# Kernel optimization log

Hardware: AMD Instinct MI355X
Metric: run time of the kernel (lower is better)

Reference implementation:

```python
import jax, jax.numpy as jnp
import numpy as np

SCALES = (0, 1, 2, 3)
SIGMA_NSQ = 2.0
SIGMA_MAX_INV = 4.0 / (255.0 * 255.0)
GAIN_LIMIT = 100.0  # NEG=False
EPS = 1e-10


def gaussian_kernel_2d(N):
    sigma = N / 5.0
    x = jnp.arange(N, dtype=jnp.float32) - (N - 1) / 2.0
    g = jnp.exp(-(x * x) / (2.0 * sigma * sigma))
    k = jnp.outer(g, g)
    return (k / jnp.sum(k))[None, None]  # [1,1,N,N]


def reflect_pad(x, p):
    return jnp.pad(x, ((0, 0), (0, 0), (p, p), (p, p)), mode='reflect')


def conv2d(x, w, stride=1, groups=1):
    return jax.lax.conv_general_dilated(
        x, w, (stride, stride), 'VALID',
        dimension_numbers=('NCHW', 'OIHW', 'NCHW'),
        feature_group_count=groups)


def vif_num_den(ref, dist):
    ref = ref - 128.0
    dist = dist - 128.0
    h, w = ref.shape[-2], ref.shape[-1]
    nums, dens = [], []
    for scale in SCALES:
        N = 2 ** (4 - scale) + 1
        win = gaussian_kernel_2d(N)
        p = (N - 1) // 2
        if scale > 0:
            h, w = h // 2, w // 2
            ref = conv2d(reflect_pad(ref, p), win, stride=2)[:, :, :h, :w]
            dist = conv2d(reflect_pad(dist, p), win, stride=2)[:, :, :h, :w]
        win5 = jnp.tile(win, (5, 1, 1, 1))  # grouped conv, 5 channels
        inp = jnp.concatenate([ref, dist, ref * ref, dist * dist, ref * dist], axis=1)
        out = conv2d(reflect_pad(inp, p), win5, groups=5)  # [b,5,h,w]
        mu1, mu2, s1, s2, s12 = [out[:, i:i + 1] for i in range(5)]
        s1 = jax.nn.relu(s1 - mu1 * mu1)
        s2 = jax.nn.relu(s2 - mu2 * mu2)
        s12 = s12 - mu1 * mu2
        g = s12 / (s1 + EPS)
        sv = s2 - g * s12
        m1 = s1 < EPS
        g = jnp.where(m1, 0.0, g)
        sv = jnp.where(m1, s2, sv)
        s1 = jnp.where(m1, 0.0, s1)
        m2 = s2 < EPS
        g = jnp.where(m2, 0.0, g)
        sv = jnp.where(m2, 0.0, sv)
        sv = jnp.where(g < 0.0, s2, sv)
        g = jax.nn.relu(g)
        sv = jnp.where(sv <= EPS, EPS, sv)
        g = jnp.minimum(g, GAIN_LIMIT)
        num_ar = jnp.log2(1.0 + g * g * s1 / (sv + SIGMA_NSQ))
        den_ar = jnp.log2(1.0 + s1 / SIGMA_NSQ)
        num_ar = jnp.where(s12 < 0.0, 0.0, num_ar)
        m3 = s1 < SIGMA_NSQ
        num_ar = jnp.where(m3, 1.0 - s2 * SIGMA_MAX_INV, num_ar)
        den_ar = jnp.where(m3, 1.0, den_ar)
        nums.append(jnp.sum(num_ar, axis=(-1, -2, -3)))
        dens.append(jnp.sum(den_ar, axis=(-1, -2, -3)))
    return jnp.stack(nums, axis=-1), jnp.stack(dens, axis=-1)


def setup_inputs() -> dict:
    key = jax.random.key(0)
    k1, k2 = jax.random.split(key)
    shape = (4, 1, 1080, 1920)
    ref = jax.random.uniform(k1, shape, dtype=jnp.float32) * 255.0
    dist = jax.random.uniform(k2, shape, dtype=jnp.float32) * 255.0
    return {"ref": ref, "dist": dist}


def reference(ref, dist):
    num, den = vif_num_den(ref, dist)
    return num / den  # VIF features per scale, shape [b, 4]
```

## Files before the change

kernel.cpp:

```cpp
#include <hip/hip_runtime.h>
#include <math.h>

#define VIF_EPS       1e-10f
#define SIGMA_NSQ     2.0f
#define SIGMA_MAX_INV (4.0f / (255.0f * 255.0f))
#define GAIN_LIMIT    100.0f

typedef float v2f __attribute__((ext_vector_type(2)));
typedef float v4f __attribute__((ext_vector_type(4)));

static __device__ __forceinline__ v2f splat2(float s) {
    v2f v; v.x = s; v.y = s; return v;
}

__device__ __forceinline__ int reflect_idx(int i, int n) {
    i = (i < 0) ? -i : i;
    i = (i >= n) ? (2 * n - 2 - i) : i;
    return i;
}

template <int N>
__device__ __forceinline__ void compute_weights(float* wts) {
    if (threadIdx.x == 0) {
        const float sigma = (float)N / 5.0f;
        const float denom = 2.0f * sigma * sigma;
        float s = 0.0f;
        for (int i = 0; i < N; ++i) {
            float x = (float)i - (float)(N - 1) * 0.5f;
            float g = expf(-(x * x) / denom);
            wts[i] = g;
            s += g;
        }
        for (int i = 0; i < N; ++i) wts[i] = wts[i] / s;
    }
}

constexpr int tile_w(int N) { return (128 - (N - 1)) & ~3; }

template <int N>
struct alignas(16) StatsSmem {
    v2f   a[8][132];
    v2f   bq[8][132];
    float c[8][132];
    float wts[N];
    float rsum[8];
};
template <int N>
struct alignas(16) DownSmem {
    v2f vb[8][252];
    float wts[N];
};

template <int N>
__device__ __forceinline__ void stats_body(
    StatsSmem<N>& sm, const float* __restrict__ refp, const float* __restrict__ distp,
    int h, int w, float shift, double2* __restrict__ partial,
    int sy, int sx, int bx, int b) {
    constexpr int P   = (N - 1) / 2;
    constexpr int VC  = 128;
    constexpr int TW  = tile_w(N);
    constexpr int TH  = 8;
    constexpr int Q   = 4;
    constexpr int LR  = Q + 2 * P;
    constexpr int XG  = TW / 4;

    const int tid = threadIdx.x;
    const int ytile = bx % sy;
    const int xtile = bx / sy;
    const int x0 = xtile * TW;
    const int y0 = ytile * TH;

    compute_weights<N>(sm.wts);
    __syncthreads();

    float wr[N];
#pragma unroll
    for (int j = 0; j < N; ++j) wr[j] = sm.wts[j];

    {
        const int cc = tid & (VC - 1);
        const int g  = tid >> 7;
        const int gx = reflect_idx(x0 + cc - P, w);
        const float* rb = refp  + (size_t)b * h * w + gx;
        const float* db = distp + (size_t)b * h * w + gx;

        v2f accA[Q], accB[Q];
        float accC[Q];
#pragma unroll
        for (int q = 0; q < Q; ++q) {
            accA[q] = splat2(0.f);
            accB[q] = splat2(0.f);
            accC[q] = 0.f;
        }

        auto acc_push = [&](int i, float r, float d) {
            v2f rd; rd.x = r; rd.y = d;
            v2f sq = rd * rd;
            float x = r * d;
#pragma unroll
            for (int q = 0; q < Q; ++q) {
                const int j = i - q;
                if (j >= 0 && j < N) {
                    const float wj = wr[j];
                    accA[q] += splat2(wj) * rd;
                    accB[q] += splat2(wj) * sq;
                    accC[q] += wj * x;
                }
            }
        };

        const int rowlo = y0 + g * Q - P;
        if (rowlo >= 0 && rowlo + LR <= h) {
            const float* pr = rb + (size_t)rowlo * w;
            const float* pd = db + (size_t)rowlo * w;
#pragma unroll
            for (int i = 0; i < LR; ++i) {
                float r = pr[0] - shift;
                float d = pd[0] - shift;
                pr += w; pd += w;
                acc_push(i, r, d);
            }
        } else {
#pragma unroll
            for (int i = 0; i < LR; ++i) {
                int gy = reflect_idx(rowlo + i, h);
                float r = rb[(size_t)gy * w] - shift;
                float d = db[(size_t)gy * w] - shift;
                acc_push(i, r, d);
            }
        }
#pragma unroll
        for (int q = 0; q < Q; ++q) {
            sm.a[g * Q + q][cc]  = accA[q];
            sm.bq[g * Q + q][cc] = accB[q];
            sm.c[g * Q + q][cc]  = accC[q];
        }
    }
    __syncthreads();

    float num_v = 0.f, den_v = 0.f;
    {
        const int xg  = tid & 31;
        const int row = tid >> 5;
        if (xg < XG) {
            constexpr int WC  = N + 3;
            constexpr int F4C = (WC + 3) / 4;

            v2f muA[4], muB[4];
            float muC[4];
#pragma unroll
            for (int q = 0; q < 4; ++q) {
                muA[q] = splat2(0.f);
                muB[q] = splat2(0.f);
                muC[q] = 0.f;
            }

            const v4f* A4 = (const v4f*)&sm.a[row][xg * 4];
            const v4f* B4 = (const v4f*)&sm.bq[row][xg * 4];
#pragma unroll
            for (int f = 0; f < WC / 2; ++f) {
                v4f ta = A4[f];
                v4f tb = B4[f];
#pragma unroll
                for (int hlf = 0; hlf < 2; ++hlf) {
                    const int k = 2 * f + hlf;
                    v2f pa = hlf ? __builtin_shufflevector(ta, ta, 2, 3)
                                 : __builtin_shufflevector(ta, ta, 0, 1);
                    v2f pb = hlf ? __builtin_shufflevector(tb, tb, 2, 3)
                                 : __builtin_shufflevector(tb, tb, 0, 1);
#pragma unroll
                    for (int q = 0; q < 4; ++q) {
                        const int j = k - q;
                        if (j >= 0 && j < N) {
                            const float wj = wr[j];
                            muA[q] += splat2(wj) * pa;
                            muB[q] += splat2(wj) * pb;
                        }
                    }
                }
            }
            {
                const v4f* C4 = (const v4f*)&sm.c[row][xg * 4];
#pragma unroll
                for (int f = 0; f < F4C; ++f) {
                    v4f t = C4[f];
#pragma unroll
                    for (int e = 0; e < 4; ++e) {
                        const int k = 4 * f + e;
                        const float x = (e == 0) ? t.x : (e == 1) ? t.y
                                      : (e == 2) ? t.z : t.w;
#pragma unroll
                        for (int q = 0; q < 4; ++q) {
                            const int j = k - q;
                            if (j >= 0 && j < N) muC[q] += wr[j] * x;
                        }
                    }
                }
            }

            const int gy = y0 + row;
#pragma unroll
            for (int q = 0; q < 4; ++q) {
                int gx = x0 + xg * 4 + q;
                if (gx < w && gy < h) {
                    float mu1 = muA[q].x, mu2 = muA[q].y;
                    float s1  = fmaxf(0.f, muB[q].x - mu1 * mu1);
                    float s2  = fmaxf(0.f, muB[q].y - mu2 * mu2);
                    float s12 = muC[q] - mu1 * mu2;

                    float g  = s12 / (s1 + VIF_EPS);
                    float sv = s2 - g * s12;
                    if (s1 < VIF_EPS) { g = 0.f; sv = s2; s1 = 0.f; }
                    if (s2 < VIF_EPS) { g = 0.f; sv = 0.f; }
                    if (g  < 0.f)     { sv = s2; g = 0.f; }
                    if (sv <= VIF_EPS) sv = VIF_EPS;
                    g = fminf(g, GAIN_LIMIT);

                    float num_ar = __log2f(1.f + g * g * s1 / (sv + SIGMA_NSQ));
                    float den_ar = __log2f(1.f + s1 / SIGMA_NSQ);
                    if (s12 < 0.f) num_ar = 0.f;
                    if (s1 < SIGMA_NSQ) { num_ar = 1.f - s2 * SIGMA_MAX_INV; den_ar = 1.f; }
                    num_v += num_ar;
                    den_v += den_ar;
                }
            }
        }
    }

#pragma unroll
    for (int off = 32; off > 0; off >>= 1) {
        num_v += __shfl_down(num_v, off);
        den_v += __shfl_down(den_v, off);
    }
    const int wid = tid >> 6, lane = tid & 63;
    if (lane == 0) { sm.rsum[wid] = num_v; sm.rsum[4 + wid] = den_v; }
    __syncthreads();
    if (tid == 0) {
        float ns = sm.rsum[0] + sm.rsum[1] + sm.rsum[2] + sm.rsum[3];
        float ds = sm.rsum[4] + sm.rsum[5] + sm.rsum[6] + sm.rsum[7];
        partial[(size_t)b * (sy * sx) + bx] = make_double2((double)ns, (double)ds);
    }
}

template <int N>
__device__ __forceinline__ void down_body(
    DownSmem<N>& sm, const float* __restrict__ rin, const float* __restrict__ din,
    float* __restrict__ rout, float* __restrict__ dout,
    int h, int w, int h2, int w2, float shift, int dgx, int bx, int b) {
    constexpr int P   = (N - 1) / 2;
    constexpr int TOW = 120, TOH = 8;
    constexpr int IC  = 2 * (TOW - 1) + N;
    constexpr int NR  = 2 * (TOH - 1) + N;
    constexpr int XG4 = TOW / 4;
    constexpr int WL  = N + 6;

    compute_weights<N>(sm.wts);
    __syncthreads();

    float wr[N];
#pragma unroll
    for (int j = 0; j < N; ++j) wr[j] = sm.wts[j];

    const int tid = threadIdx.x;
    const int xt  = bx % dgx;
    const int yt  = bx / dgx;
    const int x0  = xt * TOW;
    const int y0  = yt * TOH;

    if (tid < IC) {
        const int gx = reflect_idx(2 * x0 - P + tid, w);
        const int rowlo = 2 * y0 - P;
        const float* rb = rin + (size_t)b * h * w + gx;
        const float* db = din + (size_t)b * h * w + gx;

        v2f acc[TOH];
#pragma unroll
        for (int t = 0; t < TOH; ++t) acc[t] = splat2(0.f);

        const bool interior = (rowlo >= 0) && (rowlo + NR <= h);
        if (interior) {
            const float* pr = rb + (size_t)rowlo * w;
            const float* pd = db + (size_t)rowlo * w;
#pragma unroll
            for (int i = 0; i < NR; ++i) {
                v2f x; x.x = pr[0] - shift; x.y = pd[0] - shift;
                pr += w; pd += w;
#pragma unroll
                for (int t = 0; t < TOH; ++t) {
                    const int j = i - 2 * t;
                    if (j >= 0 && j < N) acc[t] += splat2(wr[j]) * x;
                }
            }
        } else {
#pragma unroll
            for (int i = 0; i < NR; ++i) {
                const int gy = reflect_idx(rowlo + i, h);
                v2f x; x.x = rb[(size_t)gy * w] - shift; x.y = db[(size_t)gy * w] - shift;
#pragma unroll
                for (int t = 0; t < TOH; ++t) {
                    const int j = i - 2 * t;
                    if (j >= 0 && j < N) acc[t] += splat2(wr[j]) * x;
                }
            }
        }
#pragma unroll
        for (int t = 0; t < TOH; ++t) sm.vb[t][tid] = acc[t];
    }
    __syncthreads();

    if (tid < TOH * XG4) {
        const int row = tid / XG4;
        const int xg  = tid - row * XG4;

        v2f o[4];
#pragma unroll
        for (int q = 0; q < 4; ++q) o[q] = splat2(0.f);

        const v4f* s4 = (const v4f*)&sm.vb[row][8 * xg];
#pragma unroll
        for (int f = 0; f < (WL + 1) / 2; ++f) {
            v4f t = s4[f];
#pragma unroll
            for (int hlf = 0; hlf < 2; ++hlf) {
                const int k = 2 * f + hlf;
                v2f p = hlf ? __builtin_shufflevector(t, t, 2, 3)
                            : __builtin_shufflevector(t, t, 0, 1);
#pragma unroll
                for (int q = 0; q < 4; ++q) {
                    const int j = k - 2 * q;
                    if (j >= 0 && j < N) o[q] += splat2(wr[j]) * p;
                }
            }
        }
        const int gy = y0 + row;
        if (gy < h2) {
            float* rp = rout + (size_t)b * h2 * w2 + (size_t)gy * w2 + x0 + 4 * xg;
            float* dp = dout + (size_t)b * h2 * w2 + (size_t)gy * w2 + x0 + 4 * xg;
            *(float4*)rp = make_float4(o[0].x, o[1].x, o[2].x, o[3].x);
            *(float4*)dp = make_float4(o[0].y, o[1].y, o[2].y, o[3].y);
        }
    }
}

template <int NS, int ND>
__global__ __launch_bounds__(256) void fused_kernel(
    const float* __restrict__ sref, const float* __restrict__ sdist,
    int sh, int sw, float sshift, double2* __restrict__ partial, int sy, int sx,
    float* __restrict__ drout, float* __restrict__ ddout,
    int dh2, int dw2, int dgx, int nStats) {
    __shared__ union {
        StatsSmem<NS> s;
        DownSmem<ND>  d;
    } u;
    const int bx = blockIdx.x;
    const int b  = blockIdx.z;
    if (bx < nStats)
        stats_body<NS>(u.s, sref, sdist, sh, sw, sshift, partial, sy, sx, bx, b);
    else
        down_body<ND>(u.d, sref, sdist, drout, ddout, sh, sw, dh2, dw2, sshift, dgx,
                      bx - nStats, b);
}

template <int N>
__global__ __launch_bounds__(256) void stats_only_kernel(
    const float* __restrict__ refp, const float* __restrict__ distp,
    int h, int w, float shift, double2* __restrict__ partial, int sy, int sx) {
    __shared__ StatsSmem<N> sm;
    stats_body<N>(sm, refp, distp, h, w, shift, partial, sy, sx, blockIdx.x, blockIdx.z);
}

__global__ __launch_bounds__(256) void reduce_kernel(
    const double2* __restrict__ part, float* __restrict__ out,
    int4 bases, int4 counts) {
    __shared__ double sn[4], sd[4];
    const int s = blockIdx.x & 3;
    const int b = blockIdx.x >> 2;
    const int base = (&bases.x)[s];
    const int cnt  = (&counts.x)[s];
    const double2* p = part + base + (size_t)b * cnt;

    double ns = 0.0, ds = 0.0;
    for (int i = threadIdx.x; i < cnt; i += 256) {
        double2 v = p[i];
        ns += v.x;
        ds += v.y;
    }
#pragma unroll
    for (int off = 32; off > 0; off >>= 1) {
        ns += __shfl_down(ns, off);
        ds += __shfl_down(ds, off);
    }
    const int wid = threadIdx.x >> 6, lane = threadIdx.x & 63;
    if (lane == 0) { sn[wid] = ns; sd[wid] = ds; }
    __syncthreads();
    if (threadIdx.x == 0) {
        double Nv = sn[0] + sn[1] + sn[2] + sn[3];
        double Dv = sd[0] + sd[1] + sd[2] + sd[3];
        out[b * 4 + s] = (float)(Nv / Dv);
    }
}

extern "C" void kernel_launch(void* const* d_in, const int* in_sizes, int n_in,
                              void* d_out, int out_size, void* d_ws, size_t ws_size,
                              hipStream_t stream) {
    const float* ref  = (const float*)d_in[0];
    const float* dist = (const float*)d_in[1];
    float* out = (float*)d_out;

    const int B = 4;
    const int H0 = 1080, W0 = 1920;
    const int H1 = 540,  W1 = 960;
    const int H2 = 270,  W2 = 480;
    const int H3 = 135,  W3 = 240;

    char*  ws  = (char*)d_ws;
    size_t off = 0;
    auto alloc = [&](size_t bytes) -> void* {
        void* p = ws + off;
        off += (bytes + 255) & ~(size_t)255;
        return p;
    };
    float* ref1  = (float*)alloc((size_t)B * H1 * W1 * 4);
    float* dist1 = (float*)alloc((size_t)B * H1 * W1 * 4);
    float* ref2  = (float*)alloc((size_t)B * H2 * W2 * 4);
    float* dist2 = (float*)alloc((size_t)B * H2 * W2 * 4);
    float* ref3  = (float*)alloc((size_t)B * H3 * W3 * 4);
    float* dist3 = (float*)alloc((size_t)B * H3 * W3 * 4);

    const int sx0 = (W0 + tile_w(17) - 1) / tile_w(17), sy0 = (H0 + 7) / 8;
    const int sx1 = (W1 + tile_w(9)  - 1) / tile_w(9),  sy1 = (H1 + 7) / 8;
    const int sx2 = (W2 + tile_w(5)  - 1) / tile_w(5),  sy2 = (H2 + 7) / 8;
    const int sx3 = (W3 + tile_w(3)  - 1) / tile_w(3),  sy3 = (H3 + 7) / 8;
    const int n0 = sx0 * sy0, n1 = sx1 * sy1, n2 = sx2 * sy2, n3 = sx3 * sy3;

    const int dgx1 = W1 / 120, nD1 = dgx1 * ((H1 + 7) / 8);
    const int dgx2 = W2 / 120, nD2 = dgx2 * ((H2 + 7) / 8);
    const int dgx3 = W3 / 120, nD3 = dgx3 * ((H3 + 7) / 8);

    double2* part = (double2*)alloc((size_t)B * (n0 + n1 + n2 + n3) * sizeof(double2));
    double2* p0 = part;
    double2* p1 = p0 + (size_t)B * n0;
    double2* p2 = p1 + (size_t)B * n1;
    double2* p3 = p2 + (size_t)B * n2;

    dim3 blk(256);

    fused_kernel<17, 9><<<dim3(n0 + nD1, 1, B), blk, 0, stream>>>(
        ref, dist, H0, W0, 128.0f, p0, sy0, sx0,
        ref1, dist1, H1, W1, dgx1, n0);

    fused_kernel<9, 5><<<dim3(n1 + nD2, 1, B), blk, 0, stream>>>(
        ref1, dist1, H1, W1, 0.0f, p1, sy1, sx1,
        ref2, dist2, H2, W2, dgx2, n1);

    fused_kernel<5, 3><<<dim3(n2 + nD3, 1, B), blk, 0, stream>>>(
        ref2, dist2, H2, W2, 0.0f, p2, sy2, sx2,
        ref3, dist3, H3, W3, dgx3, n2);

    stats_only_kernel<3><<<dim3(n3, 1, B), blk, 0, stream>>>(
        ref3, dist3, H3, W3, 0.0f, p3, sy3, sx3);

    reduce_kernel<<<16, 256, 0, stream>>>(
        part, out,
        make_int4(0, B * n0, B * (n0 + n1), B * (n0 + n1 + n2)),
        make_int4(n0, n1, n2, n3));
}
```

Measured before the change: 193.3 us.

## Widen stats tile to 256 columns with one thread per column over all rows

The stats kernel's tile grows from 128 to 256 columns. Each of the 256 threads now runs the vertical pass for one column across all 8 output rows, where before two row-groups of 4 each re-read their own halo rows. This cuts redundant global halo loads per tile, both vertically and horizontally, at the cost of more accumulator registers and larger shared memory. The horizontal pass loops over tasks when they exceed 256, and global addressing switches to 32-bit byte offsets from a base pointer in both kernels so the loads can use cheaper offset arithmetic.

Result: faster. 188.2 us (-2.6%).

```diff
diff --git a/kernel.cpp b/kernel.cpp
--- a/kernel.cpp
+++ b/kernel.cpp
@@ -35,13 +35,13 @@
     }
 }
 
-constexpr int tile_w(int N) { return (128 - (N - 1)) & ~3; }
+constexpr int tile_w(int N) { return (256 - (N - 1)) & ~3; }
 
 template <int N>
 struct alignas(16) StatsSmem {
-    v2f   a[8][132];
-    v2f   bq[8][132];
-    float c[8][132];
+    v2f   a[8][258];
+    v2f   bq[8][258];
+    float c[8][260];
     float wts[N];
     float rsum[8];
 };
@@ -57,12 +57,12 @@
     int h, int w, float shift, double2* __restrict__ partial,
     int sy, int sx, int bx, int b) {
     constexpr int P   = (N - 1) / 2;
-    constexpr int VC  = 128;
     constexpr int TW  = tile_w(N);
     constexpr int TH  = 8;
-    constexpr int Q   = 4;
-    constexpr int LR  = Q + 2 * P;
-    constexpr int XG  = TW / 4;
+    constexpr int LR  = TH + 2 * P;
+    constexpr int XG4 = TW / 4;
+    constexpr int NT  = TH * XG4;
+    constexpr int REPS = (NT + 255) / 256;
 
     const int tid = threadIdx.x;
     const int ytile = bx % sy;
@@ -78,19 +78,18 @@
     for (int j = 0; j < N; ++j) wr[j] = sm.wts[j];
 
     {
-        const int cc = tid & (VC - 1);
-        const int g  = tid >> 7;
+        const int cc = tid;
         const int gx = reflect_idx(x0 + cc - P, w);
-        const float* rb = refp  + (size_t)b * h * w + gx;
-        const float* db = distp + (size_t)b * h * w + gx;
-
-        v2f accA[Q], accB[Q];
-        float accC[Q];
-#pragma unroll
-        for (int q = 0; q < Q; ++q) {
-            accA[q] = splat2(0.f);
-            accB[q] = splat2(0.f);
-            accC[q] = 0.f;
+        const float* rbase = refp  + (size_t)b * h * w;
+        const float* dbase = distp + (size_t)b * h * w;
+
+        v2f accA[TH], accB[TH];
+        float accC[TH];
+#pragma unroll
+        for (int t = 0; t < TH; ++t) {
+            accA[t] = splat2(0.f);
+            accB[t] = splat2(0.f);
+            accC[t] = 0.f;
         }
 
         auto acc_push = [&](int i, float r, float d) {
@@ -98,130 +97,135 @@
             v2f sq = rd * rd;
             float x = r * d;
 #pragma unroll
-            for (int q = 0; q < Q; ++q) {
-                const int j = i - q;
+            for (int t = 0; t < TH; ++t) {
+                const int j = i - t;
                 if (j >= 0 && j < N) {
                     const float wj = wr[j];
-                    accA[q] += splat2(wj) * rd;
-                    accB[q] += splat2(wj) * sq;
-                    accC[q] += wj * x;
+                    accA[t] += splat2(wj) * rd;
+                    accB[t] += splat2(wj) * sq;
+                    accC[t] += wj * x;
                 }
             }
         };
 
-        const int rowlo = y0 + g * Q - P;
+        const int rowlo = y0 - P;
         if (rowlo >= 0 && rowlo + LR <= h) {
-            const float* pr = rb + (size_t)rowlo * w;
-            const float* pd = db + (size_t)rowlo * w;
+            unsigned voff = (unsigned)(rowlo * w + gx) * 4u;
+            const unsigned vstep = (unsigned)w * 4u;
 #pragma unroll
             for (int i = 0; i < LR; ++i) {
-                float r = pr[0] - shift;
-                float d = pd[0] - shift;
-                pr += w; pd += w;
+                float r = *(const float*)((const char*)rbase + voff) - shift;
+                float d = *(const float*)((const char*)dbase + voff) - shift;
+                voff += vstep;
                 acc_push(i, r, d);
             }
         } else {
 #pragma unroll
             for (int i = 0; i < LR; ++i) {
-                int gy = reflect_idx(rowlo + i, h);
-                float r = rb[(size_t)gy * w] - shift;
-                float d = db[(size_t)gy * w] - shift;
+                const int gy = reflect_idx(rowlo + i, h);
+                const size_t o = (size_t)gy * w + gx;
+                float r = rbase[o] - shift;
+                float d = dbase[o] - shift;
                 acc_push(i, r, d);
             }
         }
 #pragma unroll
-        for (int q = 0; q < Q; ++q) {
-            sm.a[g * Q + q][cc]  = accA[q];
-            sm.bq[g * Q + q][cc] = accB[q];
-            sm.c[g * Q + q][cc]  = accC[q];
+        for (int t = 0; t < TH; ++t) {
+            sm.a[t][cc]  = accA[t];
+            sm.bq[t][cc] = accB[t];
+            sm.c[t][cc]  = accC[t];
         }
     }
     __syncthreads();
 
     float num_v = 0.f, den_v = 0.f;
     {
-        const int xg  = tid & 31;
-        const int row = tid >> 5;
-        if (xg < XG) {
-            constexpr int WC  = N + 3;
-            constexpr int F4C = (WC + 3) / 4;
-
-            v2f muA[4], muB[4];
-            float muC[4];
-#pragma unroll
-            for (int q = 0; q < 4; ++q) {
-                muA[q] = splat2(0.f);
-                muB[q] = splat2(0.f);
-                muC[q] = 0.f;
-            }
-
-            const v4f* A4 = (const v4f*)&sm.a[row][xg * 4];
-            const v4f* B4 = (const v4f*)&sm.bq[row][xg * 4];
-#pragma unroll
-            for (int f = 0; f < WC / 2; ++f) {
-                v4f ta = A4[f];
-                v4f tb = B4[f];
-#pragma unroll
-                for (int hlf = 0; hlf < 2; ++hlf) {
-                    const int k = 2 * f + hlf;
-                    v2f pa = hlf ? __builtin_shufflevector(ta, ta, 2, 3)
-                                 : __builtin_shufflevector(ta, ta, 0, 1);
-                    v2f pb = hlf ? __builtin_shufflevector(tb, tb, 2, 3)
-                                 : __builtin_shufflevector(tb, tb, 0, 1);
-#pragma unroll
-                    for (int q = 0; q < 4; ++q) {
-                        const int j = k - q;
-                        if (j >= 0 && j < N) {
-                            const float wj = wr[j];
-                            muA[q] += splat2(wj) * pa;
-                            muB[q] += splat2(wj) * pb;
+        constexpr int WC  = N + 3;
+        constexpr int F4C = (WC + 3) / 4;
+#pragma unroll
+        for (int rep = 0; rep < REPS; ++rep) {
+            const int task = tid + 256 * rep;
+            if (task < NT) {
+                const int row = task / XG4;
+                const int xg  = task - row * XG4;
+
+                v2f muA[4], muB[4];
+                float muC[4];
+#pragma unroll
+                for (int q = 0; q < 4; ++q) {
+                    muA[q] = splat2(0.f);
+                    muB[q] = splat2(0.f);
+                    muC[q] = 0.f;
+                }
+
+                const v4f* A4 = (const v4f*)&sm.a[row][xg * 4];
+                const v4f* B4 = (const v4f*)&sm.bq[row][xg * 4];
+#pragma unroll
+                for (int f = 0; f < WC / 2; ++f) {
+                    v4f ta = A4[f];
+                    v4f tb = B4[f];
+#pragma unroll
+                    for (int hlf = 0; hlf < 2; ++hlf) {
+                        const int k = 2 * f + hlf;
+                        v2f pa = hlf ? __builtin_shufflevector(ta, ta, 2, 3)
+                                     : __builtin_shufflevector(ta, ta, 0, 1);
+                        v2f pb = hlf ? __builtin_shufflevector(tb, tb, 2, 3)
+                                     : __builtin_shufflevector(tb, tb, 0, 1);
+#pragma unroll
+                        for (int q = 0; q < 4; ++q) {
+                            const int j = k - q;
+                            if (j >= 0 && j < N) {
+                                const float wj = wr[j];
+                                muA[q] += splat2(wj) * pa;
+                                muB[q] += splat2(wj) * pb;
+                            }
                         }
                     }
                 }
-            }
-            {
-                const v4f* C4 = (const v4f*)&sm.c[row][xg * 4];
-#pragma unroll
-                for (int f = 0; f < F4C; ++f) {
-                    v4f t = C4[f];
-#pragma unroll
-                    for (int e = 0; e < 4; ++e) {
-                        const int k = 4 * f + e;
-                        const float x = (e == 0) ? t.x : (e == 1) ? t.y
-                                      : (e == 2) ? t.z : t.w;
-#pragma unroll
-                        for (int q = 0; q < 4; ++q) {
-                            const int j = k - q;
-                            if (j >= 0 && j < N) muC[q] += wr[j] * x;
+                {
+                    const v4f* C4 = (const v4f*)&sm.c[row][xg * 4];
+#pragma unroll
+                    for (int f = 0; f < F4C; ++f) {
+                        v4f t = C4[f];
+#pragma unroll
+                        for (int e = 0; e < 4; ++e) {
+                            const int k = 4 * f + e;
+                            const float x = (e == 0) ? t.x : (e == 1) ? t.y
+                                          : (e == 2) ? t.z : t.w;
+#pragma unroll
+                            for (int q = 0; q < 4; ++q) {
+                                const int j = k - q;
+                                if (j >= 0 && j < N) muC[q] += wr[j] * x;
+                            }
                         }
                     }
                 }
-            }
-
-            const int gy = y0 + row;
-#pragma unroll
-            for (int q = 0; q < 4; ++q) {
-                int gx = x0 + xg * 4 + q;
-                if (gx < w && gy < h) {
-                    float mu1 = muA[q].x, mu2 = muA[q].y;
-                    float s1  = fmaxf(0.f, muB[q].x - mu1 * mu1);
-                    float s2  = fmaxf(0.f, muB[q].y - mu2 * mu2);
-                    float s12 = muC[q] - mu1 * mu2;
-
-                    float g  = s12 / (s1 + VIF_EPS);
-                    float sv = s2 - g * s12;
-                    if (s1 < VIF_EPS) { g = 0.f; sv = s2; s1 = 0.f; }
-                    if (s2 < VIF_EPS) { g = 0.f; sv = 0.f; }
-                    if (g  < 0.f)     { sv = s2; g = 0.f; }
-                    if (sv <= VIF_EPS) sv = VIF_EPS;
-                    g = fminf(g, GAIN_LIMIT);
-
-                    float num_ar = __log2f(1.f + g * g * s1 / (sv + SIGMA_NSQ));
-                    float den_ar = __log2f(1.f + s1 / SIGMA_NSQ);
-                    if (s12 < 0.f) num_ar = 0.f;
-                    if (s1 < SIGMA_NSQ) { num_ar = 1.f - s2 * SIGMA_MAX_INV; den_ar = 1.f; }
-                    num_v += num_ar;
-                    den_v += den_ar;
+
+                const int gy = y0 + row;
+#pragma unroll
+                for (int q = 0; q < 4; ++q) {
+                    int gx = x0 + xg * 4 + q;
+                    if (gx < w && gy < h) {
+                        float mu1 = muA[q].x, mu2 = muA[q].y;
+                        float s1  = fmaxf(0.f, muB[q].x - mu1 * mu1);
+                        float s2  = fmaxf(0.f, muB[q].y - mu2 * mu2);
+                        float s12 = muC[q] - mu1 * mu2;
+
+                        float g  = s12 / (s1 + VIF_EPS);
+                        float sv = s2 - g * s12;
+                        if (s1 < VIF_EPS) { g = 0.f; sv = s2; s1 = 0.f; }
+                        if (s2 < VIF_EPS) { g = 0.f; sv = 0.f; }
+                        if (g  < 0.f)     { sv = s2; g = 0.f; }
+                        if (sv <= VIF_EPS) sv = VIF_EPS;
+                        g = fminf(g, GAIN_LIMIT);
+
+                        float num_ar = __log2f(1.f + g * g * s1 / (sv + SIGMA_NSQ));
+                        float den_ar = __log2f(1.f + s1 / SIGMA_NSQ);
+                        if (s12 < 0.f) num_ar = 0.f;
+                        if (s1 < SIGMA_NSQ) { num_ar = 1.f - s2 * SIGMA_MAX_INV; den_ar = 1.f; }
+                        num_v += num_ar;
+                        den_v += den_ar;
+                    }
                 }
             }
         }
@@ -270,8 +274,8 @@
     if (tid < IC) {
         const int gx = reflect_idx(2 * x0 - P + tid, w);
         const int rowlo = 2 * y0 - P;
-        const float* rb = rin + (size_t)b * h * w + gx;
-        const float* db = din + (size_t)b * h * w + gx;
+        const float* rbase = rin + (size_t)b * h * w;
+        const float* dbase = din + (size_t)b * h * w;
 
         v2f acc[TOH];
 #pragma unroll
@@ -279,12 +283,14 @@
 
         const bool interior = (rowlo >= 0) && (rowlo + NR <= h);
         if (interior) {
-            const float* pr = rb + (size_t)rowlo * w;
-            const float* pd = db + (size_t)rowlo * w;
+            unsigned voff = (unsigned)(rowlo * w + gx) * 4u;
+            const unsigned vstep = (unsigned)w * 4u;
 #pragma unroll
             for (int i = 0; i < NR; ++i) {
-                v2f x; x.x = pr[0] - shift; x.y = pd[0] - shift;
-                pr += w; pd += w;
+                v2f x;
+                x.x = *(const float*)((const char*)rbase + voff) - shift;
+                x.y = *(const float*)((const char*)dbase + voff) - shift;
+                voff += vstep;
 #pragma unroll
                 for (int t = 0; t < TOH; ++t) {
                     const int j = i - 2 * t;
@@ -295,7 +301,8 @@
 #pragma unroll
             for (int i = 0; i < NR; ++i) {
                 const int gy = reflect_idx(rowlo + i, h);
-                v2f x; x.x = rb[(size_t)gy * w] - shift; x.y = db[(size_t)gy * w] - shift;
+                const size_t o = (size_t)gy * w + gx;
+                v2f x; x.x = rbase[o] - shift; x.y = dbase[o] - shift;
 #pragma unroll
                 for (int t = 0; t < TOH; ++t) {
                     const int j = i - 2 * t;
```
